# Kernel tuning notes

Hardware: AMD Instinct MI355X
Metric: run time of the kernel (lower is better)

The kernel has to match this reference:

```python
import jax, jax.numpy as jnp
import numpy as np

KM_ITERS = 20  # fixed Lloyd iterations (scipy kmeans iterates to tolerance with random init;
               # we use deterministic min/max init so centroid 0 = dark, 1 = bright)


def _kmeans_mask(img2d):
    """2-means clustering of pixel intensities of one [H,W] image + border-vote flip."""
    H, W = img2d.shape
    x = img2d.reshape(-1)  # [N]
    c0 = jnp.stack([x.min(), x.max()])  # deterministic init: centroid0=min, centroid1=max

    def step(c, _):
        code = jnp.argmin(jnp.abs(x[:, None] - c[None, :]), axis=1)  # [N] in {0,1}
        one = code == 1
        n1 = jnp.sum(one)
        n0 = x.shape[0] - n1
        s1 = jnp.sum(jnp.where(one, x, jnp.zeros_like(x)))
        s0 = jnp.sum(x) - s1
        c_new = jnp.stack([s0 / jnp.maximum(n0, 1).astype(x.dtype),
                           s1 / jnp.maximum(n1, 1).astype(x.dtype)])
        return c_new, None

    c, _ = jax.lax.scan(step, c0, None, length=KM_ITERS)
    # final assignment (scipy vq step)
    code = jnp.argmin(jnp.abs(x[:, None] - c[None, :]), axis=1).reshape(H, W)

    # border vote: if >=3 borders are mostly cluster-1, flip so text region is 1
    fc = code[:, 0].sum()
    lc = code[:, -1].sum()
    fr = code[0, :].sum()
    lr = code[-1, :].sum()
    num = ((fr > W // 2).astype(jnp.int32) + (lr > W // 2).astype(jnp.int32)
           + (fc > H // 2).astype(jnp.int32) + (lc > H // 2).astype(jnp.int32))
    mask = jnp.where(num >= 3, 1 - code, code)
    return mask.astype(img2d.dtype)


def get_mask(img_tensor):
    gray = img_tensor.mean(axis=1)  # [B,H,W]
    # clustering is non-differentiable in the original (runs on detached CPU numpy)
    masks = jax.vmap(_kmeans_mask)(jax.lax.stop_gradient(gray))
    return masks[:, None, :, :]  # [B,1,H,W]


def setup_inputs() -> dict:
    key = jax.random.key(0)
    k1, k2 = jax.random.split(key)
    B, C, H, W = 128, 3, 256, 256
    hr_img = jax.random.uniform(k1, (B, C, H, W), dtype=jnp.float32)
    sr_mask = jax.random.uniform(k2, (B, 1, H, W), dtype=jnp.float32)
    return {"hr_img": hr_img, "sr_mask": sr_mask}


def reference(hr_img, sr_mask):
    hr_mask = get_mask(hr_img)  # same spatial size -> no interpolation branch
    return jnp.mean((sr_mask - hr_mask) ** 2)
```

## Files before the change

kernel.cpp:

```cpp
#include <hip/hip_runtime.h>


constexpr int NB   = 2048;
constexpr int NPIX = 65536;
constexpr int KM_ITERS = 20;
constexpr float QINV  = 1.0f / 65536.0f;
constexpr float BINW  = 1.0f / 2048.0f;

constexpr size_t OFF_MINENC = 0;
constexpr size_t OFF_MAXU   = 512;
constexpr size_t OFF_TINFO  = 1024;
constexpr size_t OFF_BORD   = 3072;
constexpr size_t OFF_HCNT   = 8192;
constexpr size_t OFF_GRAY   = OFF_HCNT + (size_t)128 * NB * 4;
constexpr size_t OFF_BSUM   = OFF_GRAY + (size_t)128 * NPIX * 2;
constexpr size_t MEMSET_BYTES = OFF_GRAY;

__device__ __forceinline__ float waveSumF(float v) {
#pragma unroll
    for (int off = 32; off > 0; off >>= 1) v += __shfl_down(v, off, 64);
    return v;
}
__device__ __forceinline__ unsigned waveMinU(unsigned v) {
#pragma unroll
    for (int off = 32; off > 0; off >>= 1) v = min(v, (unsigned)__shfl_down((int)v, off, 64));
    return v;
}
__device__ __forceinline__ unsigned waveMaxU(unsigned v) {
#pragma unroll
    for (int off = 32; off > 0; off >>= 1) v = max(v, (unsigned)__shfl_down((int)v, off, 64));
    return v;
}

__global__ __launch_bounds__(256) void kA_hist(
        const float* __restrict__ hr, unsigned* __restrict__ minenc,
        unsigned* __restrict__ maxu, unsigned* __restrict__ hcnt,
        ushort* __restrict__ gray) {
    const int img = blockIdx.x >> 3, part = blockIdx.x & 7, tid = threadIdx.x;
    const int lane = tid & 63, wid = tid >> 6;

    __shared__ unsigned hcL[NB];
    __shared__ unsigned smn[4], smx[4];
    for (int j = tid; j < NB; j += 256) hcL[j] = 0u;
    __syncthreads();

    const float* r = hr + (size_t)img * 3 * NPIX;
    const float* g = r + NPIX;
    const float* b = g + NPIX;
    ushort* gp = gray + (size_t)img * NPIX;

    unsigned umn = 65535u, umx = 0u;
#pragma unroll
    for (int i = 0; i < 8; ++i) {
        const int p = part * 8192 + i * 1024 + tid * 4;
        float4 rr = *(const float4*)(r + p);
        float4 gg = *(const float4*)(g + p);
        float4 bb = *(const float4*)(b + p);
        float x[4] = { (rr.x + gg.x + bb.x) * (1.0f / 3.0f),
                       (rr.y + gg.y + bb.y) * (1.0f / 3.0f),
                       (rr.z + gg.z + bb.z) * (1.0f / 3.0f),
                       (rr.w + gg.w + bb.w) * (1.0f / 3.0f) };
        unsigned u[4];
#pragma unroll
        for (int j = 0; j < 4; ++j) {
            unsigned uu = (unsigned)(x[j] * 65536.0f);
            uu = min(uu, 65535u);
            u[j] = uu;
            umn = min(umn, uu); umx = max(umx, uu);
            atomicAdd(&hcL[uu >> 5], 1u);
        }
        ushort4 u4;
        u4.x = (ushort)u[0]; u4.y = (ushort)u[1];
        u4.z = (ushort)u[2]; u4.w = (ushort)u[3];
        *(ushort4*)(gp + p) = u4;
    }
    __syncthreads();

    for (int j = tid; j < NB; j += 256) {
        const unsigned c = hcL[j];
        if (c) atomicAdd(&hcnt[(size_t)img * NB + j], c);
    }

    umn = waveMinU(umn); umx = waveMaxU(umx);
    if (lane == 0) { smn[wid] = umn; smx[wid] = umx; }
    __syncthreads();
    if (tid == 0) {
        const unsigned bmn = min(min(smn[0], smn[1]), min(smn[2], smn[3]));
        const unsigned bmx = max(max(smx[0], smx[1]), max(smx[2], smx[3]));
        atomicMax(&maxu[img], bmx);
        atomicMax(&minenc[img], 65535u - bmn);
    }
}

__global__ __launch_bounds__(256) void kB_lloyd(
        const unsigned* __restrict__ minenc, const unsigned* __restrict__ maxu,
        const unsigned* __restrict__ hcnt, float4* __restrict__ tinfo) {
    const int img = blockIdx.x, tid = threadIdx.x;
    __shared__ float sN[NB + 1], sS[NB + 1];
    __shared__ float tN[256], tS[256];

    const int base = tid * 8;
    float n8[8], s8[8];
#pragma unroll
    for (int u = 0; u < 8; ++u) {
        const float c = (float)hcnt[(size_t)img * NB + base + u];
        n8[u] = c;
        s8[u] = c * (((float)(base + u) + 0.484375f) * BINW);
    }
    float accN = 0.0f, accS = 0.0f;
#pragma unroll
    for (int u = 7; u >= 0; --u) {
        accN += n8[u]; n8[u] = accN;
        accS += s8[u]; s8[u] = accS;
    }
    tN[tid] = accN; tS[tid] = accS;
    __syncthreads();
    for (int off = 1; off < 256; off <<= 1) {
        float aN = 0.0f, aS = 0.0f;
        if (tid + off < 256) { aN = tN[tid + off]; aS = tS[tid + off]; }
        __syncthreads();
        tN[tid] += aN; tS[tid] += aS;
        __syncthreads();
    }
    const float exN = (tid < 255) ? tN[tid + 1] : 0.0f;
    const float exS = (tid < 255) ? tS[tid + 1] : 0.0f;
#pragma unroll
    for (int u = 0; u < 8; ++u) { sN[base + u] = n8[u] + exN; sS[base + u] = s8[u] + exS; }
    if (tid == 0) { sN[NB] = 0.0f; sS[NB] = 0.0f; }
    __syncthreads();

    if (tid == 0) {
        float c0 = (float)(65535u - minenc[img]) * QINV;
        float c1 = (float)maxu[img] * QINV;
        const float Stot = sS[0];
        const float Ntot = (float)NPIX;
#pragma unroll 1
        for (int it = 0; it < KM_ITERS; ++it) {
            const float t = 0.5f * (c0 + c1);
            float n1, s1;
            if (c1 == c0) { n1 = 0.0f; s1 = 0.0f; }
            else {
                const float f = t * (float)NB;
                int k = (int)floorf(f);
                k = max(0, min(NB - 1, k));
                float frac = (float)(k + 1) - f;
                frac = fminf(fmaxf(frac, 0.0f), 1.0f);
                const float cntk = sN[k] - sN[k + 1];
                const float aN = sN[k + 1] + cntk * frac;
                const float aS = sS[k + 1] +
                                 cntk * frac * 0.5f * (t + (float)(k + 1) * BINW);
                if (c1 > c0) { n1 = aN; s1 = aS; }
                else         { n1 = Ntot - aN; s1 = Stot - aS; }
            }
            const float c1n = s1 / fmaxf(n1, 1.0f);
            const float c0n = (Stot - s1) / fmaxf(Ntot - n1, 1.0f);
            if (c1n == c1 && c0n == c0) break;
            c0 = c0n; c1 = c1n;
        }
        float tf, hii;
        if (c1 == c0) { tf = -1e30f; hii = 0.0f; }
        else { tf = 0.5f * (c0 + c1); hii = (c1 > c0) ? 1.0f : 0.0f; }
        tinfo[img] = make_float4(tf, hii, 0.0f, 0.0f);
    }
}

__global__ __launch_bounds__(256) void kC_mse(
        const ushort* __restrict__ gray, const float* __restrict__ sr,
        const float4* __restrict__ tinfo, unsigned* __restrict__ bord,
        float2* __restrict__ bsum) {
    const int img = blockIdx.x >> 3, part = blockIdx.x & 7, tid = threadIdx.x;
    const int lane = tid & 63, wid = tid >> 6;
    __shared__ float sA0[4], sA1[4];
    __shared__ float4 sB[4];

    const float4 ti = tinfo[img];
    const float t = ti.x;
    const bool hi = (ti.y != 0.0f);

    const ushort* gp = gray + (size_t)img * NPIX;
    const float*  sp = sr   + (size_t)img * NPIX;

    float a0 = 0.0f, a1 = 0.0f;
    float fr = 0.0f, lr = 0.0f, fc = 0.0f, lc = 0.0f;
#pragma unroll
    for (int i = 0; i < 8; ++i) {
        const int p = part * 8192 + i * 1024 + tid * 4;
        ushort4 u4 = *(const ushort4*)(gp + p);
        float4  ss = *(const float4*)(sp + p);
        const unsigned uu[4] = { u4.x, u4.y, u4.z, u4.w };
        const float    sv[4] = { ss.x, ss.y, ss.z, ss.w };
        const int row = p >> 8;
#pragma unroll
        for (int j = 0; j < 4; ++j) {
            const float x = (float)uu[j] * QINV;
            const bool one = hi ? (x > t) : (x < t);
            const float m = one ? 1.0f : 0.0f;
            const float d0 = sv[j] - m;
            const float d1 = sv[j] - (1.0f - m);
            a0 += d0 * d0;
            a1 += d1 * d1;
            const int col = (p & 255) + j;
            if (col == 0)   fc += m;
            if (col == 255) lc += m;
            if (row == 0)   fr += m;
            if (row == 255) lr += m;
        }
    }
    a0 = waveSumF(a0); a1 = waveSumF(a1);
    fr = waveSumF(fr); lr = waveSumF(lr); fc = waveSumF(fc); lc = waveSumF(lc);
    if (lane == 0) { sA0[wid] = a0; sA1[wid] = a1; sB[wid] = make_float4(fr, lr, fc, lc); }
    __syncthreads();
    if (tid == 0) {
        bsum[blockIdx.x] = make_float2(sA0[0] + sA0[1] + sA0[2] + sA0[3],
                                       sA1[0] + sA1[1] + sA1[2] + sA1[3]);
        const float FR = sB[0].x + sB[1].x + sB[2].x + sB[3].x;
        const float LR = sB[0].y + sB[1].y + sB[2].y + sB[3].y;
        const float FC = sB[0].z + sB[1].z + sB[2].z + sB[3].z;
        const float LC = sB[0].w + sB[1].w + sB[2].w + sB[3].w;
        unsigned* bb = bord + (size_t)img * 4;
        if (FR > 0.5f) atomicAdd(&bb[0], (unsigned)(FR + 0.5f));
        if (LR > 0.5f) atomicAdd(&bb[1], (unsigned)(LR + 0.5f));
        if (FC > 0.5f) atomicAdd(&bb[2], (unsigned)(FC + 0.5f));
        if (LC > 0.5f) atomicAdd(&bb[3], (unsigned)(LC + 0.5f));
    }
}

__global__ __launch_bounds__(256) void kD_final(
        const unsigned* __restrict__ bord, const float2* __restrict__ bsum,
        float* __restrict__ out) {
    const int tid = threadIdx.x, lane = tid & 63, wid = tid >> 6;
    __shared__ float flipS[128];
    __shared__ float sm[4];
    if (tid < 128) {
        const unsigned* bb = bord + (size_t)tid * 4;
        const int num = (bb[0] > 128u) + (bb[1] > 128u) + (bb[2] > 128u) + (bb[3] > 128u);
        flipS[tid] = (num >= 3) ? 1.0f : 0.0f;
    }
    __syncthreads();
    float acc = 0.0f;
#pragma unroll
    for (int q = 0; q < 4; ++q) {
        const int e = tid * 4 + q;
        const float2 v = bsum[e];
        acc += (flipS[e >> 3] != 0.0f) ? v.y : v.x;
    }
    acc = waveSumF(acc);
    if (lane == 0) sm[wid] = acc;
    __syncthreads();
    if (tid == 0) out[0] = (sm[0] + sm[1] + sm[2] + sm[3]) * (1.0f / 8388608.0f);
}

extern "C" void kernel_launch(void* const* d_in, const int* in_sizes, int n_in,
                              void* d_out, int out_size, void* d_ws, size_t ws_size,
                              hipStream_t stream) {
    const float* hr = (const float*)d_in[0];
    const float* sr = (const float*)d_in[1];
    float* out = (float*)d_out;

    char* ws = (char*)d_ws;
    unsigned* minenc = (unsigned*)(ws + OFF_MINENC);
    unsigned* maxu   = (unsigned*)(ws + OFF_MAXU);
    float4*   tinfo  = (float4*)(ws + OFF_TINFO);
    unsigned* bord   = (unsigned*)(ws + OFF_BORD);
    unsigned* hcnt   = (unsigned*)(ws + OFF_HCNT);
    ushort*   gray   = (ushort*)(ws + OFF_GRAY);
    float2*   bsum   = (float2*)(ws + OFF_BSUM);

    hipMemsetAsync(d_ws, 0, MEMSET_BYTES, stream);
    kA_hist <<<1024, 256, 0, stream>>>(hr, minenc, maxu, hcnt, gray);
    kB_lloyd<<< 128, 256, 0, stream>>>(minenc, maxu, hcnt, tinfo);
    kC_mse  <<<1024, 256, 0, stream>>>(gray, sr, tinfo, bord, bsum);
    kD_final<<<   1, 256, 0, stream>>>(bord, bsum, out);
}
```

Baseline: 189.3 us.

## Fuse mask-loss pipeline into one cooperative kernel keeping gray in registers

Replaces the memset and four separate kernels with a single cooperative-groups kernel using grid-wide syncs. Quantized gray values stay in registers between the histogram and MSE phases, so the gray buffer is never written to or read from global memory. Per-block sub-histograms and min/max are written without atomics, so no memset is needed. The Lloyd iterations now run across the whole block with wave reductions instead of a single thread over a prefix-summed histogram. In exchange it adds grid.sync barriers, a 32-register array per thread, and host-side occupancy and attribute queries on every launch, with a multi-kernel fallback if cooperative launch is unavailable.

```diff
diff --git a/kernel.cpp b/kernel.cpp
--- a/kernel.cpp
+++ b/kernel.cpp
@@ -1,20 +1,29 @@
 #include <hip/hip_runtime.h>
+#include <hip/hip_cooperative_groups.h>
+
+namespace cg = cooperative_groups;
 
 
 constexpr int NB   = 2048;
 constexpr int NPIX = 65536;
 constexpr int KM_ITERS = 20;
-constexpr float QINV  = 1.0f / 65536.0f;
-constexpr float BINW  = 1.0f / 2048.0f;
-
-constexpr size_t OFF_MINENC = 0;
-constexpr size_t OFF_MAXU   = 512;
-constexpr size_t OFF_TINFO  = 1024;
-constexpr size_t OFF_BORD   = 3072;
-constexpr size_t OFF_HCNT   = 8192;
-constexpr size_t OFF_GRAY   = OFF_HCNT + (size_t)128 * NB * 4;
-constexpr size_t OFF_BSUM   = OFF_GRAY + (size_t)128 * NPIX * 2;
-constexpr size_t MEMSET_BYTES = OFF_GRAY;
+constexpr int GRID = 512, TPB = 256, BPI = 4;
+constexpr int PXB  = 16384;
+constexpr float QINV = 1.0f / 65536.0f;
+constexpr float BINW = 1.0f / 2048.0f;
+
+constexpr size_t OFF_BMM   = 0;
+constexpr size_t OFF_TINFO = 4096;
+constexpr size_t OFF_BSUM  = 8192;
+constexpr size_t OFF_BBORD = 16384;
+constexpr size_t OFF_SUBH  = 32768;
+constexpr size_t OFF_GRAY  = OFF_SUBH + (size_t)GRID * NB * 4;
+
+struct ShA { unsigned hc[NB]; unsigned mn[4]; unsigned mx[4]; };
+struct ShB { float w1[4]; float w2[4]; };
+struct ShC { float a0[4]; float a1[4]; float4 bd[4]; };
+struct ShD { float flip[128]; float sm[4]; };
+union ShU { ShA a; ShB b; ShC c; ShD d; };
 
 __device__ __forceinline__ float waveSumF(float v) {
 #pragma unroll
@@ -32,27 +41,21 @@
     return v;
 }
 
-__global__ __launch_bounds__(256) void kA_hist(
-        const float* __restrict__ hr, unsigned* __restrict__ minenc,
-        unsigned* __restrict__ maxu, unsigned* __restrict__ hcnt,
-        ushort* __restrict__ gray) {
-    const int img = blockIdx.x >> 3, part = blockIdx.x & 7, tid = threadIdx.x;
-    const int lane = tid & 63, wid = tid >> 6;
-
-    __shared__ unsigned hcL[NB];
-    __shared__ unsigned smn[4], smx[4];
-    for (int j = tid; j < NB; j += 256) hcL[j] = 0u;
-    __syncthreads();
-
+template<bool COOP>
+__device__ __forceinline__ void phaseA(int bid, int tid, const float* __restrict__ hr,
+        uint2* __restrict__ bmm, unsigned* __restrict__ subh,
+        ushort* __restrict__ gray, unsigned* g16, ShA& sh) {
+    const int img = bid >> 2, part = bid & 3, lane = tid & 63, wid = tid >> 6;
+    for (int j = tid; j < NB; j += TPB) sh.hc[j] = 0u;
+    __syncthreads();
     const float* r = hr + (size_t)img * 3 * NPIX;
     const float* g = r + NPIX;
     const float* b = g + NPIX;
-    ushort* gp = gray + (size_t)img * NPIX;
-
+    ushort* gp = gray ? (gray + (size_t)img * NPIX) : nullptr;
     unsigned umn = 65535u, umx = 0u;
 #pragma unroll
-    for (int i = 0; i < 8; ++i) {
-        const int p = part * 8192 + i * 1024 + tid * 4;
+    for (int i = 0; i < 16; ++i) {
+        const int p = part * PXB + i * 1024 + tid * 4;
         float4 rr = *(const float4*)(r + p);
         float4 gg = *(const float4*)(g + p);
         float4 bb = *(const float4*)(b + p);
@@ -67,96 +70,85 @@
             uu = min(uu, 65535u);
             u[j] = uu;
             umn = min(umn, uu); umx = max(umx, uu);
-            atomicAdd(&hcL[uu >> 5], 1u);
-        }
-        ushort4 u4;
-        u4.x = (ushort)u[0]; u4.y = (ushort)u[1];
-        u4.z = (ushort)u[2]; u4.w = (ushort)u[3];
-        *(ushort4*)(gp + p) = u4;
-    }
-    __syncthreads();
-
-    for (int j = tid; j < NB; j += 256) {
-        const unsigned c = hcL[j];
-        if (c) atomicAdd(&hcnt[(size_t)img * NB + j], c);
-    }
-
+            atomicAdd(&sh.hc[uu >> 5], 1u);
+        }
+        if constexpr (COOP) {
+            g16[2 * i]     = u[0] | (u[1] << 16);
+            g16[2 * i + 1] = u[2] | (u[3] << 16);
+        } else {
+            ushort4 u4;
+            u4.x = (ushort)u[0]; u4.y = (ushort)u[1];
+            u4.z = (ushort)u[2]; u4.w = (ushort)u[3];
+            *(ushort4*)(gp + p) = u4;
+        }
+    }
     umn = waveMinU(umn); umx = waveMaxU(umx);
-    if (lane == 0) { smn[wid] = umn; smx[wid] = umx; }
+    if (lane == 0) { sh.mn[wid] = umn; sh.mx[wid] = umx; }
     __syncthreads();
     if (tid == 0) {
-        const unsigned bmn = min(min(smn[0], smn[1]), min(smn[2], smn[3]));
-        const unsigned bmx = max(max(smx[0], smx[1]), max(smx[2], smx[3]));
-        atomicMax(&maxu[img], bmx);
-        atomicMax(&minenc[img], 65535u - bmn);
-    }
-}
-
-__global__ __launch_bounds__(256) void kB_lloyd(
-        const unsigned* __restrict__ minenc, const unsigned* __restrict__ maxu,
-        const unsigned* __restrict__ hcnt, float4* __restrict__ tinfo) {
-    const int img = blockIdx.x, tid = threadIdx.x;
-    __shared__ float sN[NB + 1], sS[NB + 1];
-    __shared__ float tN[256], tS[256];
-
-    const int base = tid * 8;
-    float n8[8], s8[8];
+        bmm[bid] = make_uint2(min(min(sh.mn[0], sh.mn[1]), min(sh.mn[2], sh.mn[3])),
+                              max(max(sh.mx[0], sh.mx[1]), max(sh.mx[2], sh.mx[3])));
+    }
+    unsigned* ho = subh + (size_t)bid * NB;
+    for (int j = tid; j < NB; j += TPB) ho[j] = sh.hc[j];
+}
+
+__device__ __forceinline__ void phaseB(int img, int tid, const uint2* __restrict__ bmm,
+        const unsigned* __restrict__ subh, float4* __restrict__ tinfo, ShB& sh) {
+    const int lane = tid & 63, wid = tid >> 6, base = tid * 8;
+    float n8[8], c8[8];
 #pragma unroll
     for (int u = 0; u < 8; ++u) {
-        const float c = (float)hcnt[(size_t)img * NB + base + u];
-        n8[u] = c;
-        s8[u] = c * (((float)(base + u) + 0.484375f) * BINW);
-    }
-    float accN = 0.0f, accS = 0.0f;
-#pragma unroll
-    for (int u = 7; u >= 0; --u) {
-        accN += n8[u]; n8[u] = accN;
-        accS += s8[u]; s8[u] = accS;
-    }
-    tN[tid] = accN; tS[tid] = accS;
-    __syncthreads();
-    for (int off = 1; off < 256; off <<= 1) {
+        const unsigned* hp = subh + (size_t)(img * BPI) * NB + (base + u);
+        const unsigned c = hp[0] + hp[NB] + hp[2 * NB] + hp[3 * NB];
+        n8[u] = (float)c;
+        c8[u] = ((float)(base + u) + 0.484375f) * BINW;
+    }
+    float pS = 0.0f;
+#pragma unroll
+    for (int u = 0; u < 8; ++u) pS += n8[u] * c8[u];
+    pS = waveSumF(pS);
+    if (lane == 0) sh.w1[wid] = pS;
+    __syncthreads();
+    const float Stot = sh.w1[0] + sh.w1[1] + sh.w1[2] + sh.w1[3];
+    const float Ntot = (float)NPIX;
+    const uint2 m0 = bmm[img * BPI], m1 = bmm[img * BPI + 1],
+                m2 = bmm[img * BPI + 2], m3 = bmm[img * BPI + 3];
+    float c0 = (float)min(min(m0.x, m1.x), min(m2.x, m3.x)) * QINV;
+    float c1 = (float)max(max(m0.y, m1.y), max(m2.y, m3.y)) * QINV;
+    __syncthreads();
+#pragma unroll 1
+    for (int it = 0; it < KM_ITERS; ++it) {
+        const float t = 0.5f * (c0 + c1);
         float aN = 0.0f, aS = 0.0f;
-        if (tid + off < 256) { aN = tN[tid + off]; aS = tS[tid + off]; }
+        if (c1 != c0) {
+#pragma unroll
+            for (int u = 0; u < 8; ++u) {
+                const float bs = (float)(base + u) * BINW, be = bs + BINW;
+                if (t <= bs) { aN += n8[u]; aS += n8[u] * c8[u]; }
+                else if (t < be) {
+                    const float fr = (be - t) * (float)NB;
+                    aN += n8[u] * fr;
+                    aS += n8[u] * fr * 0.5f * (t + be);
+                }
+            }
+        }
+        aN = waveSumF(aN); aS = waveSumF(aS);
+        if (lane == 0) { sh.w1[wid] = aN; sh.w2[wid] = aS; }
         __syncthreads();
-        tN[tid] += aN; tS[tid] += aS;
+        const float AN = sh.w1[0] + sh.w1[1] + sh.w1[2] + sh.w1[3];
+        const float AS = sh.w2[0] + sh.w2[1] + sh.w2[2] + sh.w2[3];
+        float n1, s1;
+        if (c1 == c0)      { n1 = 0.0f;       s1 = 0.0f; }
+        else if (c1 > c0)  { n1 = AN;         s1 = AS; }
+        else               { n1 = Ntot - AN;  s1 = Stot - AS; }
+        const float c1n = s1 / fmaxf(n1, 1.0f);
+        const float c0n = (Stot - s1) / fmaxf(Ntot - n1, 1.0f);
         __syncthreads();
-    }
-    const float exN = (tid < 255) ? tN[tid + 1] : 0.0f;
-    const float exS = (tid < 255) ? tS[tid + 1] : 0.0f;
-#pragma unroll
-    for (int u = 0; u < 8; ++u) { sN[base + u] = n8[u] + exN; sS[base + u] = s8[u] + exS; }
-    if (tid == 0) { sN[NB] = 0.0f; sS[NB] = 0.0f; }
-    __syncthreads();
-
+        if (c1n == c1 && c0n == c0) break;
+        c0 = c0n; c1 = c1n;
+    }
     if (tid == 0) {
-        float c0 = (float)(65535u - minenc[img]) * QINV;
-        float c1 = (float)maxu[img] * QINV;
-        const float Stot = sS[0];
-        const float Ntot = (float)NPIX;
-#pragma unroll 1
-        for (int it = 0; it < KM_ITERS; ++it) {
-            const float t = 0.5f * (c0 + c1);
-            float n1, s1;
-            if (c1 == c0) { n1 = 0.0f; s1 = 0.0f; }
-            else {
-                const float f = t * (float)NB;
-                int k = (int)floorf(f);
-                k = max(0, min(NB - 1, k));
-                float frac = (float)(k + 1) - f;
-                frac = fminf(fmaxf(frac, 0.0f), 1.0f);
-                const float cntk = sN[k] - sN[k + 1];
-                const float aN = sN[k + 1] + cntk * frac;
-                const float aS = sS[k + 1] +
-                                 cntk * frac * 0.5f * (t + (float)(k + 1) * BINW);
-                if (c1 > c0) { n1 = aN; s1 = aS; }
-                else         { n1 = Ntot - aN; s1 = Stot - aS; }
-            }
-            const float c1n = s1 / fmaxf(n1, 1.0f);
-            const float c0n = (Stot - s1) / fmaxf(Ntot - n1, 1.0f);
-            if (c1n == c1 && c0n == c0) break;
-            c0 = c0n; c1 = c1n;
-        }
         float tf, hii;
         if (c1 == c0) { tf = -1e30f; hii = 0.0f; }
         else { tf = 0.5f * (c0 + c1); hii = (c1 > c0) ? 1.0f : 0.0f; }
@@ -164,32 +156,32 @@
     }
 }
 
-__global__ __launch_bounds__(256) void kC_mse(
+template<bool COOP>
+__device__ __forceinline__ void phaseC(int bid, int tid, const unsigned* g16,
         const ushort* __restrict__ gray, const float* __restrict__ sr,
-        const float4* __restrict__ tinfo, unsigned* __restrict__ bord,
-        float2* __restrict__ bsum) {
-    const int img = blockIdx.x >> 3, part = blockIdx.x & 7, tid = threadIdx.x;
-    const int lane = tid & 63, wid = tid >> 6;
-    __shared__ float sA0[4], sA1[4];
-    __shared__ float4 sB[4];
-
+        const float4* __restrict__ tinfo, float2* __restrict__ bsum,
+        float4* __restrict__ bbord, ShC& sh) {
+    const int img = bid >> 2, part = bid & 3, lane = tid & 63, wid = tid >> 6;
     const float4 ti = tinfo[img];
     const float t = ti.x;
     const bool hi = (ti.y != 0.0f);
-
-    const ushort* gp = gray + (size_t)img * NPIX;
-    const float*  sp = sr   + (size_t)img * NPIX;
-
-    float a0 = 0.0f, a1 = 0.0f;
-    float fr = 0.0f, lr = 0.0f, fc = 0.0f, lc = 0.0f;
-#pragma unroll
-    for (int i = 0; i < 8; ++i) {
-        const int p = part * 8192 + i * 1024 + tid * 4;
-        ushort4 u4 = *(const ushort4*)(gp + p);
-        float4  ss = *(const float4*)(sp + p);
-        const unsigned uu[4] = { u4.x, u4.y, u4.z, u4.w };
-        const float    sv[4] = { ss.x, ss.y, ss.z, ss.w };
+    const float* sp = sr + (size_t)img * NPIX;
+    const ushort* gp = gray ? (gray + (size_t)img * NPIX) : nullptr;
+    float a0 = 0.0f, a1 = 0.0f, frr = 0.0f, lrr = 0.0f, fcc = 0.0f, lcc = 0.0f;
+#pragma unroll
+    for (int i = 0; i < 16; ++i) {
+        const int p = part * PXB + i * 1024 + tid * 4;
+        float4 ss = *(const float4*)(sp + p);
+        unsigned uu[4];
+        if constexpr (COOP) {
+            uu[0] = g16[2 * i] & 0xFFFFu;     uu[1] = g16[2 * i] >> 16;
+            uu[2] = g16[2 * i + 1] & 0xFFFFu; uu[3] = g16[2 * i + 1] >> 16;
+        } else {
+            ushort4 u4 = *(const ushort4*)(gp + p);
+            uu[0] = u4.x; uu[1] = u4.y; uu[2] = u4.z; uu[3] = u4.w;
+        }
         const int row = p >> 8;
+        const float sv[4] = { ss.x, ss.y, ss.z, ss.w };
 #pragma unroll
         for (int j = 0; j < 4; ++j) {
             const float x = (float)uu[j] * QINV;
@@ -200,54 +192,97 @@
             a0 += d0 * d0;
             a1 += d1 * d1;
             const int col = (p & 255) + j;
-            if (col == 0)   fc += m;
-            if (col == 255) lc += m;
-            if (row == 0)   fr += m;
-            if (row == 255) lr += m;
+            if (col == 0)   fcc += m;
+            if (col == 255) lcc += m;
+            if (row == 0)   frr += m;
+            if (row == 255) lrr += m;
         }
     }
     a0 = waveSumF(a0); a1 = waveSumF(a1);
-    fr = waveSumF(fr); lr = waveSumF(lr); fc = waveSumF(fc); lc = waveSumF(lc);
-    if (lane == 0) { sA0[wid] = a0; sA1[wid] = a1; sB[wid] = make_float4(fr, lr, fc, lc); }
+    frr = waveSumF(frr); lrr = waveSumF(lrr);
+    fcc = waveSumF(fcc); lcc = waveSumF(lcc);
+    if (lane == 0) {
+        sh.a0[wid] = a0; sh.a1[wid] = a1;
+        sh.bd[wid] = make_float4(frr, lrr, fcc, lcc);
+    }
     __syncthreads();
     if (tid == 0) {
-        bsum[blockIdx.x] = make_float2(sA0[0] + sA0[1] + sA0[2] + sA0[3],
-                                       sA1[0] + sA1[1] + sA1[2] + sA1[3]);
-        const float FR = sB[0].x + sB[1].x + sB[2].x + sB[3].x;
-        const float LR = sB[0].y + sB[1].y + sB[2].y + sB[3].y;
-        const float FC = sB[0].z + sB[1].z + sB[2].z + sB[3].z;
-        const float LC = sB[0].w + sB[1].w + sB[2].w + sB[3].w;
-        unsigned* bb = bord + (size_t)img * 4;
-        if (FR > 0.5f) atomicAdd(&bb[0], (unsigned)(FR + 0.5f));
-        if (LR > 0.5f) atomicAdd(&bb[1], (unsigned)(LR + 0.5f));
-        if (FC > 0.5f) atomicAdd(&bb[2], (unsigned)(FC + 0.5f));
-        if (LC > 0.5f) atomicAdd(&bb[3], (unsigned)(LC + 0.5f));
-    }
-}
-
-__global__ __launch_bounds__(256) void kD_final(
-        const unsigned* __restrict__ bord, const float2* __restrict__ bsum,
-        float* __restrict__ out) {
-    const int tid = threadIdx.x, lane = tid & 63, wid = tid >> 6;
-    __shared__ float flipS[128];
-    __shared__ float sm[4];
+        bsum[bid] = make_float2(sh.a0[0] + sh.a0[1] + sh.a0[2] + sh.a0[3],
+                                sh.a1[0] + sh.a1[1] + sh.a1[2] + sh.a1[3]);
+        bbord[bid] = make_float4(sh.bd[0].x + sh.bd[1].x + sh.bd[2].x + sh.bd[3].x,
+                                 sh.bd[0].y + sh.bd[1].y + sh.bd[2].y + sh.bd[3].y,
+                                 sh.bd[0].z + sh.bd[1].z + sh.bd[2].z + sh.bd[3].z,
+                                 sh.bd[0].w + sh.bd[1].w + sh.bd[2].w + sh.bd[3].w);
+    }
+}
+
+__device__ __forceinline__ void phaseD(int tid, const float2* __restrict__ bsum,
+        const float4* __restrict__ bbord, float* __restrict__ out, ShD& sh) {
+    const int lane = tid & 63, wid = tid >> 6;
     if (tid < 128) {
-        const unsigned* bb = bord + (size_t)tid * 4;
-        const int num = (bb[0] > 128u) + (bb[1] > 128u) + (bb[2] > 128u) + (bb[3] > 128u);
-        flipS[tid] = (num >= 3) ? 1.0f : 0.0f;
+        float FR = 0.0f, LR = 0.0f, FC = 0.0f, LC = 0.0f;
+#pragma unroll
+        for (int q = 0; q < 4; ++q) {
+            const float4 v = bbord[tid * 4 + q];
+            FR += v.x; LR += v.y; FC += v.z; LC += v.w;
+        }
+        const int num = (FR > 128.0f) + (LR > 128.0f) + (FC > 128.0f) + (LC > 128.0f);
+        sh.flip[tid] = (num >= 3) ? 1.0f : 0.0f;
     }
     __syncthreads();
     float acc = 0.0f;
 #pragma unroll
-    for (int q = 0; q < 4; ++q) {
-        const int e = tid * 4 + q;
+    for (int q = 0; q < 2; ++q) {
+        const int e = tid * 2 + q;
         const float2 v = bsum[e];
-        acc += (flipS[e >> 3] != 0.0f) ? v.y : v.x;
+        acc += (sh.flip[e >> 2] != 0.0f) ? v.y : v.x;
     }
     acc = waveSumF(acc);
-    if (lane == 0) sm[wid] = acc;
-    __syncthreads();
-    if (tid == 0) out[0] = (sm[0] + sm[1] + sm[2] + sm[3]) * (1.0f / 8388608.0f);
+    if (lane == 0) sh.sm[wid] = acc;
+    __syncthreads();
+    if (tid == 0)
+        out[0] = (sh.sm[0] + sh.sm[1] + sh.sm[2] + sh.sm[3]) * (1.0f / 8388608.0f);
+}
+
+__global__ __launch_bounds__(TPB) void coop_maskloss(
+        const float* __restrict__ hr, const float* __restrict__ sr,
+        uint2* __restrict__ bmm, unsigned* __restrict__ subh,
+        float4* __restrict__ tinfo, float2* __restrict__ bsum,
+        float4* __restrict__ bbord, float* __restrict__ out) {
+    __shared__ ShU sh;
+    const int bid = blockIdx.x, tid = threadIdx.x;
+    unsigned g16[32];
+    cg::grid_group grid = cg::this_grid();
+    phaseA<true>(bid, tid, hr, bmm, subh, nullptr, g16, sh.a);
+    grid.sync();
+    if (bid < 128) phaseB(bid, tid, bmm, subh, tinfo, sh.b);
+    grid.sync();
+    phaseC<true>(bid, tid, g16, nullptr, sr, tinfo, bsum, bbord, sh.c);
+    grid.sync();
+    if (bid == 0) phaseD(tid, bsum, bbord, out, sh.d);
+}
+
+__global__ __launch_bounds__(TPB) void fbA(const float* __restrict__ hr,
+        uint2* __restrict__ bmm, unsigned* __restrict__ subh,
+        ushort* __restrict__ gray) {
+    __shared__ ShA sh;
+    phaseA<false>(blockIdx.x, threadIdx.x, hr, bmm, subh, gray, nullptr, sh);
+}
+__global__ __launch_bounds__(TPB) void fbB(const uint2* __restrict__ bmm,
+        const unsigned* __restrict__ subh, float4* __restrict__ tinfo) {
+    __shared__ ShB sh;
+    phaseB(blockIdx.x, threadIdx.x, bmm, subh, tinfo, sh);
+}
+__global__ __launch_bounds__(TPB) void fbC(const ushort* __restrict__ gray,
+        const float* __restrict__ sr, const float4* __restrict__ tinfo,
+        float2* __restrict__ bsum, float4* __restrict__ bbord) {
+    __shared__ ShC sh;
+    phaseC<false>(blockIdx.x, threadIdx.x, nullptr, gray, sr, tinfo, bsum, bbord, sh);
+}
+__global__ __launch_bounds__(TPB) void fbD(const float2* __restrict__ bsum,
+        const float4* __restrict__ bbord, float* __restrict__ out) {
+    __shared__ ShD sh;
+    phaseD(threadIdx.x, bsum, bbord, out, sh);
 }
 
 extern "C" void kernel_launch(void* const* d_in, const int* in_sizes, int n_in,
@@ -258,17 +293,36 @@
     float* out = (float*)d_out;
 
     char* ws = (char*)d_ws;
-    unsigned* minenc = (unsigned*)(ws + OFF_MINENC);
-    unsigned* maxu   = (unsigned*)(ws + OFF_MAXU);
-    float4*   tinfo  = (float4*)(ws + OFF_TINFO);
-    unsigned* bord   = (unsigned*)(ws + OFF_BORD);
-    unsigned* hcnt   = (unsigned*)(ws + OFF_HCNT);
-    ushort*   gray   = (ushort*)(ws + OFF_GRAY);
-    float2*   bsum   = (float2*)(ws + OFF_BSUM);
-
-    hipMemsetAsync(d_ws, 0, MEMSET_BYTES, stream);
-    kA_hist <<<1024, 256, 0, stream>>>(hr, minenc, maxu, hcnt, gray);
-    kB_lloyd<<< 128, 256, 0, stream>>>(minenc, maxu, hcnt, tinfo);
-    kC_mse  <<<1024, 256, 0, stream>>>(gray, sr, tinfo, bord, bsum);
-    kD_final<<<   1, 256, 0, stream>>>(bord, bsum, out);
-}
+    uint2*    bmm   = (uint2*)(ws + OFF_BMM);
+    float4*   tinfo = (float4*)(ws + OFF_TINFO);
+    float2*   bsum  = (float2*)(ws + OFF_BSUM);
+    float4*   bbord = (float4*)(ws + OFF_BBORD);
+    unsigned* subh  = (unsigned*)(ws + OFF_SUBH);
+    ushort*   gray  = (ushort*)(ws + OFF_GRAY);
+
+    int dev = 0; hipGetDevice(&dev);
+    int coopAttr = 0;
+    hipDeviceGetAttribute(&coopAttr, hipDeviceAttributeCooperativeLaunch, dev);
+    int numCU = 0;
+    hipDeviceGetAttribute(&numCU, hipDeviceAttributeMultiprocessorCount, dev);
+    int maxb = 0;
+    hipError_t eOcc = hipOccupancyMaxActiveBlocksPerMultiprocessor(
+        &maxb, coop_maskloss, TPB, 0);
+    const bool tryCoop = (coopAttr != 0) && (eOcc == hipSuccess) &&
+                         ((long)maxb * (long)numCU >= (long)GRID);
+
+    bool done = false;
+    if (tryCoop) {
+        void* args[] = { (void*)&hr, (void*)&sr, (void*)&bmm, (void*)&subh,
+                         (void*)&tinfo, (void*)&bsum, (void*)&bbord, (void*)&out };
+        hipError_t e = hipLaunchCooperativeKernel(coop_maskloss, dim3(GRID),
+                                                  dim3(TPB), args, 0, stream);
+        done = (e == hipSuccess);
+    }
+    if (!done) {
+        fbA<<<GRID, TPB, 0, stream>>>(hr, bmm, subh, gray);
+        fbB<<<128,  TPB, 0, stream>>>(bmm, subh, tinfo);
+        fbC<<<GRID, TPB, 0, stream>>>(gray, sr, tinfo, bsum, bbord);
+        fbD<<<1,    TPB, 0, stream>>>(bsum, bbord, out);
+    }
+}
```

Measured after the change: 201.6 us. 1.07x slower.
